# Kernel optimization log

Measured on AMD Instinct MI355X. Metric: run time of the kernel, lower is better.

The kernel has to match this reference:

```python
import jax, jax.numpy as jnp
import numpy as np

B, N, F = 4, 4096, 32
NG = 14  # number of gate graph-convs in GCNLSTM_Cell with memory state


def setup_inputs() -> dict:
    key = jax.random.key(0)
    ks = jax.random.split(key, 7)
    x = jax.random.normal(ks[0], (B, N, F), jnp.float32)
    h = jax.random.normal(ks[1], (B, N, F), jnp.float32)
    c = jax.random.normal(ks[2], (B, N, F), jnp.float32)
    m = jax.random.normal(ks[3], (B, N, F), jnp.float32)
    # weighted dense adjacency, scaled so row sums are O(1)
    adj = jax.random.uniform(ks[4], (N, N), jnp.float32) / N
    # 14 WeightedGraphConv layers: Dense F -> 2F (single FeedForward layer, no relu)
    W = jax.random.normal(ks[5], (NG, F, 2 * F), jnp.float32) * (1.0 / np.sqrt(F))
    b = jnp.zeros((NG, 2 * F), jnp.float32)
    return {"x": x, "h": h, "c": c, "m": m, "adj": adj, "W": W, "b": b}


def _gcn(ax, W, b):
    # ax: [B,N,F] = adj @ state (precomputed); Dense to 2F then GLU split.
    z = ax @ W + b  # [B,N,2F]
    ls, rs = jnp.split(z, 2, axis=-1)
    return ls * jax.nn.sigmoid(rs)


def reference(x, h, c, m, adj, W, b):
    # shared graph aggregation for x and h (adj is the same for all gates)
    ax = jnp.einsum('nm,bmf->bnf', adj, x)  # [B,N,F]
    ah = jnp.einsum('nm,bmf->bnf', adj, h)

    fx = _gcn(ax, W[0], b[0]); fh = _gcn(ah, W[1], b[1])
    ix = _gcn(ax, W[2], b[2]); ih = _gcn(ah, W[3], b[3])
    cx = _gcn(ax, W[4], b[4]); ch = _gcn(ah, W[5], b[5])
    ox = _gcn(ax, W[6], b[6]); oh = _gcn(ah, W[7], b[7])

    f = jax.nn.sigmoid(fx + fh)
    i = jax.nn.sigmoid(ix + ih)
    o = jax.nn.sigmoid(ox + oh)
    c_new = f * c + i * jnp.tanh(cx + ch)
    h1 = o * jnp.tanh(c_new)

    # memory-state block (6 more graph convs on h1 and m)
    ah1 = jnp.einsum('nm,bmf->bnf', adj, h1)
    am = jnp.einsum('nm,bmf->bnf', adj, m)
    sa_ih = _gcn(ah1, W[8], b[8]);  sa_im = _gcn(am, W[9], b[9])
    sa_gh = _gcn(ah1, W[10], b[10]); sa_gm = _gcn(am, W[11], b[11])
    sa_oh = _gcn(ah1, W[12], b[12]); sa_om = _gcn(am, W[13], b[13])

    i2 = jax.nn.sigmoid(sa_ih + sa_im)
    g = jax.nn.sigmoid(sa_gh + sa_gm)
    o2 = jax.nn.sigmoid(sa_oh + sa_om)
    m_new = i2 * m + (1.0 - i2) * g
    h_new = m_new * o2
    return h_new, c_new, m_new
```

## Files before the change

### kernel.cpp

```cpp
#include <hip/hip_runtime.h>
#include <stdint.h>

typedef __attribute__((ext_vector_type(4))) float f32x4;
typedef __attribute__((ext_vector_type(8))) short s16x8;

#define BB 4
#define NN 4096
#define FF 32
#define BNF (BB*NN*FF)

static __device__ __forceinline__ float bf2f(uint16_t u) {
    union { uint32_t i; float f; } v; v.i = ((uint32_t)u) << 16; return v.f;
}
static __device__ __forceinline__ uint16_t f2bf(float f) {
    union { float f; uint32_t i; } v; v.f = f;
    uint32_t r = v.i + 0x7FFFu + ((v.i >> 16) & 1u);
    return (uint16_t)(r >> 16);
}
static __device__ __forceinline__ float sig_acc(float x) { return 1.0f / (1.0f + expf(-x)); }

__global__ __launch_bounds__(256) void cvt_adj(const float* __restrict__ a,
                                               uint16_t* __restrict__ ab)
{
    size_t i = ((size_t)blockIdx.x * 256 + threadIdx.x) * 8;
    float4 v0 = *(const float4*)(a + i);
    float4 v1 = *(const float4*)(a + i + 4);
    union { uint4 u; uint16_t e[8]; } o;
    o.e[0] = f2bf(v0.x); o.e[1] = f2bf(v0.y); o.e[2] = f2bf(v0.z); o.e[3] = f2bf(v0.w);
    o.e[4] = f2bf(v1.x); o.e[5] = f2bf(v1.y); o.e[6] = f2bf(v1.z); o.e[7] = f2bf(v1.w);
    *(uint4*)(ab + i) = o.u;
}

__global__ __launch_bounds__(256) void prep_w(const float* __restrict__ Wf,
                                              uint16_t* __restrict__ Wp)
{
    int idx = blockIdx.x * 256 + threadIdx.x;
    int g   = idx >> 11;
    int k   = (idx >> 6) & 31;
    int col = idx & 63;
    uint16_t v = f2bf(Wf[idx]);
    int gp = g >> 1;
    int sl = ((g & 1) << 2) | (k >> 3);
    int ph = sl ^ (col & 7);
    Wp[((gp * 64 + col) * 64) + ph * 8 + (k & 7)] = v;
}

__global__ __launch_bounds__(256) void pack_kernel(
    const float* __restrict__ s0, const float* __restrict__ s1,
    uint16_t* __restrict__ dst)
{
    int bid = blockIdx.x;
    int tensor = bid >> 8;
    int b = (bid >> 6) & 3;
    int ntile = bid & 63;
    const float* src = tensor ? s1 : s0;
    int n0 = ntile * 64;
    __shared__ uint16_t tl[32][65];
    int t = threadIdx.x;
    {
        int i = t >> 2, ch = t & 3;
        size_t idx = ((size_t)(b * NN + n0 + i)) * FF + ch * 8;
        float4 v0 = *(const float4*)(src + idx);
        float4 v1 = *(const float4*)(src + idx + 4);
        uint16_t e[8] = { f2bf(v0.x), f2bf(v0.y), f2bf(v0.z), f2bf(v0.w),
                          f2bf(v1.x), f2bf(v1.y), f2bf(v1.z), f2bf(v1.w) };
        #pragma unroll
        for (int k = 0; k < 8; k++) tl[ch * 8 + k][i] = e[k];
    }
    __syncthreads();
    {
        int f = t >> 3, ch = t & 7;
        union { uint4 u; uint16_t e[8]; } v;
        #pragma unroll
        for (int k = 0; k < 8; k++) v.e[k] = tl[f][ch * 8 + k];
        size_t row = (size_t)(tensor * 128 + b * 32 + f);
        *(uint4*)(dst + row * NN + n0 + ch * 8) = v.u;
    }
}

__global__ __launch_bounds__(256) void gemm_kernel(
    const void* __restrict__ Av,
    const uint16_t* __restrict__ Bt,
    float* __restrict__ part, uint16_t* __restrict__ Cb,
    int kLen, int direct, int isf32A)
{
    int mt = blockIdx.x, nt = blockIdx.y, ks = blockIdx.z;
    int m0 = mt * 128, c0 = nt * 128, k0 = ks * kLen;
    __shared__ __align__(16) uint16_t aL[128 * 32];
    __shared__ __align__(16) uint16_t bL[128 * 32];
    int t = threadIdx.x;
    int lane = t & 63, w = t >> 6;
    int wm = (w & 1) * 64, wn = (w >> 1) * 64;
    int lm = lane & 15, lk = lane >> 4;

    const uint16_t* A16 = (const uint16_t*)Av;
    const float*    Af  = (const float*)Av;

    f32x4 acc[4][4] = {};

    for (int kk = k0; kk < k0 + kLen; kk += 32) {
        union { uint4 u; uint16_t e[8]; } sa[2], sb[2];
        #pragma unroll
        for (int q = 0; q < 2; q++) {
            int pos = q * 4096 + t * 16;
            int row = pos >> 6;
            int col = (pos & 63) >> 1;
            size_t aidx = (size_t)(m0 + row) * 4096 + kk + col;
            size_t bidx = (size_t)(c0 + row) * 4096 + kk + col;
            if (!isf32A) {
                sa[q].u = *(const uint4*)(A16 + aidx);
            } else {
                union { uint4 u[2]; float f[8]; } va;
                va.u[0] = *(const uint4*)(Af + aidx);
                va.u[1] = *(const uint4*)(Af + aidx + 4);
                #pragma unroll
                for (int k = 0; k < 8; k++) sa[q].e[k] = f2bf(va.f[k]);
            }
            sb[q].u = *(const uint4*)(Bt + bidx);
        }
        #pragma unroll
        for (int q = 0; q < 2; q++) {
            int pos = q * 4096 + t * 16;
            *(uint4*)((char*)aL + pos) = sa[q].u;
            *(uint4*)((char*)bL + pos) = sb[q].u;
        }
        __syncthreads();
        s16x8 af[4], bfr[4];
        #pragma unroll
        for (int i = 0; i < 4; i++)
            af[i] = *(const s16x8*)(aL + (wm + i * 16 + lm) * 32 + lk * 8);
        #pragma unroll
        for (int j = 0; j < 4; j++)
            bfr[j] = *(const s16x8*)(bL + (wn + j * 16 + lm) * 32 + lk * 8);
        #pragma unroll
        for (int i = 0; i < 4; i++)
            #pragma unroll
            for (int j = 0; j < 4; j++)
                acc[i][j] = __builtin_amdgcn_mfma_f32_16x16x32_bf16(af[i], bfr[j], acc[i][j], 0, 0, 0);
        __syncthreads();
    }

    int r4 = (lane >> 4) * 4;
    if (direct) {
        #pragma unroll
        for (int i = 0; i < 4; i++)
            #pragma unroll
            for (int j = 0; j < 4; j++) {
                int c = c0 + wn + j * 16 + lm;
                int mr = m0 + wm + i * 16 + r4;
                union { uint2 u; uint16_t e[4]; } v;
                #pragma unroll
                for (int r = 0; r < 4; r++) v.e[r] = f2bf(acc[i][j][r]);
                *(uint2*)(Cb + (size_t)c * 4096 + mr) = v.u;
            }
    } else {
        #pragma unroll
        for (int i = 0; i < 4; i++)
            #pragma unroll
            for (int j = 0; j < 4; j++) {
                int c = c0 + wn + j * 16 + lm;
                int mr = m0 + wm + i * 16 + r4;
                *(f32x4*)(part + ((size_t)ks * 256 + c) * 4096 + mr) = acc[i][j];
            }
    }
}

__global__ __launch_bounds__(256) void fuse1_kernel(
    const float* __restrict__ part,
    const uint16_t* __restrict__ Cbi,
    const uint16_t* __restrict__ Wp,
    const float* __restrict__ bf_,
    const float* __restrict__ cf,
    float* __restrict__ cnew, uint16_t* __restrict__ S2t, int ns)
{
    __shared__ __align__(16) uint16_t WL[4 * 64 * 64];
    __shared__ __align__(16) float    AL[64 * 68];
    __shared__ __align__(16) float    BL[512];
    __shared__ __align__(16) uint16_t H1[32 * 72];

    int t = threadIdx.x;
    int b = blockIdx.x >> 6, n0 = (blockIdx.x & 63) * 64;

    {
        const uint4* src = (const uint4*)Wp;
        uint4* dst = (uint4*)WL;
        #pragma unroll
        for (int i = 0; i < 8; i++) dst[t + i * 256] = src[t + i * 256];
    }
    if (t < 128) *(float4*)(BL + t * 4) = *(const float4*)(bf_ + t * 4);

    {
        int r = t >> 2, ch = t & 3;
        size_t crow = (r < 32) ? (size_t)(b * 32 + r) : (size_t)(128 + b * 32 + (r - 32));
        f32x4 a0, a1, a2, a3;
        if (ns) {
            const float* s0p = part + crow * 4096 + n0 + ch * 16;
            a0 = *(const f32x4*)(s0p);
            a1 = *(const f32x4*)(s0p + 4);
            a2 = *(const f32x4*)(s0p + 8);
            a3 = *(const f32x4*)(s0p + 12);
            for (int ks = 1; ks < ns; ks++) {
                const float* sp = s0p + (size_t)ks * (256 * 4096);
                a0 += *(const f32x4*)(sp);
                a1 += *(const f32x4*)(sp + 4);
                a2 += *(const f32x4*)(sp + 8);
                a3 += *(const f32x4*)(sp + 12);
            }
        } else {
            const uint16_t* cp = Cbi + crow * 4096 + n0 + ch * 16;
            union { uint4 u; uint16_t e[8]; } v0, v1;
            v0.u = *(const uint4*)(cp);
            v1.u = *(const uint4*)(cp + 8);
            #pragma unroll
            for (int k = 0; k < 4; k++) {
                a0[k] = bf2f(v0.e[k]);     a1[k] = bf2f(v0.e[4 + k]);
                a2[k] = bf2f(v1.e[k]);     a3[k] = bf2f(v1.e[4 + k]);
            }
        }
        float* al = AL + r * 68 + ch * 16;
        *(f32x4*)(al) = a0; *(f32x4*)(al + 4) = a1;
        *(f32x4*)(al + 8) = a2; *(f32x4*)(al + 12) = a3;
    }
    __syncthreads();

    int lane = t & 63, w = t >> 6;
    int j = lane & 15, kg = lane >> 4;
    int r4 = kg * 4;

    float cv[2][4];
    #pragma unroll
    for (int h = 0; h < 2; h++)
        #pragma unroll
        for (int r = 0; r < 4; r++)
            cv[h][r] = cf[((size_t)(b * NN + n0 + w * 16 + r4 + r)) * FF + j + h * 16];

    s16x8 a_ax, a_ah;
    {
        int col = w * 16 + j;
        #pragma unroll
        for (int e = 0; e < 8; e++) {
            int k = kg * 8 + e;
            a_ax[e] = (short)f2bf(AL[k * 68 + col]);
            a_ah[e] = (short)f2bf(AL[(32 + k) * 68 + col]);
        }
    }

    float s[4][2][4];
    #pragma unroll
    for (int p = 0; p < 4; p++) {
        int g0 = p * 2, g1 = p * 2 + 1;
        f32x4 ac0[4] = {}, ac1[4] = {};
        #pragma unroll
        for (int ct = 0; ct < 4; ct++) {
            int col = ct * 16 + j;
            int ph0 = (kg)     ^ (col & 7);
            int ph1 = (4 + kg) ^ (col & 7);
            s16x8 b0 = *(const s16x8*)(WL + (p * 64 + col) * 64 + ph0 * 8);
            s16x8 b1 = *(const s16x8*)(WL + (p * 64 + col) * 64 + ph1 * 8);
            ac0[ct] = __builtin_amdgcn_mfma_f32_16x16x32_bf16(a_ax, b0, ac0[ct], 0, 0, 0);
            ac1[ct] = __builtin_amdgcn_mfma_f32_16x16x32_bf16(a_ah, b1, ac1[ct], 0, 0, 0);
        }
        #pragma unroll
        for (int h = 0; h < 2; h++)
            #pragma unroll
            for (int r = 0; r < 4; r++) {
                float z0l = ac0[h][r]     + BL[g0 * 64 + h * 16 + j];
                float z0r = ac0[2 + h][r] + BL[g0 * 64 + 32 + h * 16 + j];
                float z1l = ac1[h][r]     + BL[g1 * 64 + h * 16 + j];
                float z1r = ac1[2 + h][r] + BL[g1 * 64 + 32 + h * 16 + j];
                s[p][h][r] = z0l * sig_acc(z0r) + z1l * sig_acc(z1r);
            }
    }

    #pragma unroll
    for (int h = 0; h < 2; h++) {
        union { uint2 u; uint16_t e[4]; } pk;
        #pragma unroll
        for (int r = 0; r < 4; r++) {
            size_t gidx = ((size_t)(b * NN + n0 + w * 16 + r4 + r)) * FF + j + h * 16;
            float fg = sig_acc(s[0][h][r]);
            float ig = sig_acc(s[1][h][r]);
            float cc = tanhf(s[2][h][r]);
            float og = sig_acc(s[3][h][r]);
            float cn = fg * cv[h][r] + ig * cc;
            cnew[gidx] = cn;
            pk.e[r] = f2bf(og * tanhf(cn));
        }
        *(uint2*)(H1 + (j + h * 16) * 72 + w * 16 + r4) = pk.u;
    }
    __syncthreads();
    {
        int fr = t >> 3, ch = t & 7;
        uint4 v = *(const uint4*)(H1 + fr * 72 + ch * 8);
        *(uint4*)(S2t + ((size_t)(b * 32 + fr)) * NN + n0 + ch * 8) = v;
    }
}

__global__ __launch_bounds__(256) void fuse2_kernel(
    const float* __restrict__ part,
    const uint16_t* __restrict__ Cbi,
    const uint16_t* __restrict__ Wp,
    const float* __restrict__ bf_,
    const float* __restrict__ mf,
    float* __restrict__ hnew, float* __restrict__ mnew, int ns)
{
    __shared__ __align__(16) uint16_t WL[3 * 64 * 64];
    __shared__ __align__(16) float    AL[64 * 68];
    __shared__ __align__(16) float    BL[384];

    int t = threadIdx.x;
    int b = blockIdx.x >> 6, n0 = (blockIdx.x & 63) * 64;

    {
        const uint4* src = (const uint4*)(Wp + 4 * 64 * 64);
        uint4* dst = (uint4*)WL;
        #pragma unroll
        for (int i = 0; i < 6; i++) dst[t + i * 256] = src[t + i * 256];
    }
    if (t < 96) *(float4*)(BL + t * 4) = *(const float4*)(bf_ + 512 + t * 4);

    {
        int r = t >> 2, ch = t & 3;
        size_t crow = (r < 32) ? (size_t)(b * 32 + r) : (size_t)(128 + b * 32 + (r - 32));
        f32x4 a0, a1, a2, a3;
        if (ns) {
            const float* s0p = part + crow * 4096 + n0 + ch * 16;
            a0 = *(const f32x4*)(s0p);
            a1 = *(const f32x4*)(s0p + 4);
            a2 = *(const f32x4*)(s0p + 8);
            a3 = *(const f32x4*)(s0p + 12);
            for (int ks = 1; ks < ns; ks++) {
                const float* sp = s0p + (size_t)ks * (256 * 4096);
                a0 += *(const f32x4*)(sp);
                a1 += *(const f32x4*)(sp + 4);
                a2 += *(const f32x4*)(sp + 8);
                a3 += *(const f32x4*)(sp + 12);
            }
        } else {
            const uint16_t* cp = Cbi + crow * 4096 + n0 + ch * 16;
            union { uint4 u; uint16_t e[8]; } v0, v1;
            v0.u = *(const uint4*)(cp);
            v1.u = *(const uint4*)(cp + 8);
            #pragma unroll
            for (int k = 0; k < 4; k++) {
                a0[k] = bf2f(v0.e[k]);     a1[k] = bf2f(v0.e[4 + k]);
                a2[k] = bf2f(v1.e[k]);     a3[k] = bf2f(v1.e[4 + k]);
            }
        }
        float* al = AL + r * 68 + ch * 16;
        *(f32x4*)(al) = a0; *(f32x4*)(al + 4) = a1;
        *(f32x4*)(al + 8) = a2; *(f32x4*)(al + 12) = a3;
    }
    __syncthreads();

    int lane = t & 63, w = t >> 6;
    int j = lane & 15, kg = lane >> 4;
    int r4 = kg * 4;

    float mv[2][4];
    #pragma unroll
    for (int h = 0; h < 2; h++)
        #pragma unroll
        for (int r = 0; r < 4; r++)
            mv[h][r] = mf[((size_t)(b * NN + n0 + w * 16 + r4 + r)) * FF + j + h * 16];

    s16x8 a_h1, a_m;
    {
        int col = w * 16 + j;
        #pragma unroll
        for (int e = 0; e < 8; e++) {
            int k = kg * 8 + e;
            a_h1[e] = (short)f2bf(AL[k * 68 + col]);
            a_m[e]  = (short)f2bf(AL[(32 + k) * 68 + col]);
        }
    }

    float s[3][2][4];
    #pragma unroll
    for (int p = 0; p < 3; p++) {
        int g0 = p * 2, g1 = p * 2 + 1;
        f32x4 ac0[4] = {}, ac1[4] = {};
        #pragma unroll
        for (int ct = 0; ct < 4; ct++) {
            int col = ct * 16 + j;
            int ph0 = (kg)     ^ (col & 7);
            int ph1 = (4 + kg) ^ (col & 7);
            s16x8 b0 = *(const s16x8*)(WL + (p * 64 + col) * 64 + ph0 * 8);
            s16x8 b1 = *(const s16x8*)(WL + (p * 64 + col) * 64 + ph1 * 8);
            ac0[ct] = __builtin_amdgcn_mfma_f32_16x16x32_bf16(a_h1, b0, ac0[ct], 0, 0, 0);
            ac1[ct] = __builtin_amdgcn_mfma_f32_16x16x32_bf16(a_m, b1, ac1[ct], 0, 0, 0);
        }
        #pragma unroll
        for (int h = 0; h < 2; h++)
            #pragma unroll
            for (int r = 0; r < 4; r++) {
                float z0l = ac0[h][r]     + BL[g0 * 64 + h * 16 + j];
                float z0r = ac0[2 + h][r] + BL[g0 * 64 + 32 + h * 16 + j];
                float z1l = ac1[h][r]     + BL[g1 * 64 + h * 16 + j];
                float z1r = ac1[2 + h][r] + BL[g1 * 64 + 32 + h * 16 + j];
                s[p][h][r] = z0l * sig_acc(z0r) + z1l * sig_acc(z1r);
            }
    }

    #pragma unroll
    for (int h = 0; h < 2; h++)
        #pragma unroll
        for (int r = 0; r < 4; r++) {
            size_t gidx = ((size_t)(b * NN + n0 + w * 16 + r4 + r)) * FF + j + h * 16;
            float i2 = sig_acc(s[0][h][r]);
            float gg = sig_acc(s[1][h][r]);
            float o2 = sig_acc(s[2][h][r]);
            float mn = i2 * mv[h][r] + (1.0f - i2) * gg;
            mnew[gidx] = mn;
            hnew[gidx] = mn * o2;
        }
}

extern "C" void kernel_launch(void* const* d_in, const int* in_sizes, int n_in,
                              void* d_out, int out_size, void* d_ws, size_t ws_size,
                              hipStream_t stream) {
    (void)in_sizes; (void)n_in; (void)out_size;
    const float* x   = (const float*)d_in[0];
    const float* h   = (const float*)d_in[1];
    const float* c   = (const float*)d_in[2];
    const float* m   = (const float*)d_in[3];
    const float* adj = (const float*)d_in[4];
    const float* W   = (const float*)d_in[5];
    const float* bb  = (const float*)d_in[6];
    float* out = (float*)d_out;

    char* ws = (char*)d_ws;
    int haveAdjb = ws_size >= (size_t)(40u << 20);
    uint16_t* adjb = (uint16_t*)ws;
    size_t pOff = haveAdjb ? (size_t)(32u << 20) : 0;
    uint16_t* P    = (uint16_t*)(ws + pOff);
    uint16_t* Cbuf = (uint16_t*)(ws + pOff + (2u << 20));
    uint16_t* Wp   = (uint16_t*)(ws + pOff + (4u << 20));
    size_t partOff = pOff + (5u << 20);
    float* part = (float*)(ws + partOff);

    if (ws_size < (6u << 20)) return;
    size_t avail = ws_size - partOff;
    int ns = 0;
    if      (avail >= (size_t)(32u << 20)) ns = 8;
    else if (avail >= (size_t)(16u << 20)) ns = 4;
    else if (avail >= (size_t)( 8u << 20)) ns = 2;
    else if (avail >= (size_t)( 4u << 20)) ns = 1;

    const void* Agemm = haveAdjb ? (const void*)adjb : (const void*)adj;
    int isf32A = haveAdjb ? 0 : 1;

    if (haveAdjb) cvt_adj<<<8192, 256, 0, stream>>>(adj, adjb);
    prep_w<<<112, 256, 0, stream>>>(W, Wp);

    pack_kernel<<<512, 256, 0, stream>>>(x, h, P);
    if (ns) {
        gemm_kernel<<<dim3(32, 2, ns), 256, 0, stream>>>(Agemm, P, part, nullptr, 4096 / ns, 0, isf32A);
    } else {
        gemm_kernel<<<dim3(32, 2, 1), 256, 0, stream>>>(Agemm, P, nullptr, Cbuf, 4096, 1, isf32A);
    }
    fuse1_kernel<<<256, 256, 0, stream>>>(part, Cbuf, Wp, bb, c, out + BNF, P, ns);
    pack_kernel<<<256, 256, 0, stream>>>(m, m, P + (size_t)128 * NN);
    if (ns) {
        gemm_kernel<<<dim3(32, 2, ns), 256, 0, stream>>>(Agemm, P, part, nullptr, 4096 / ns, 0, isf32A);
    } else {
        gemm_kernel<<<dim3(32, 2, 1), 256, 0, stream>>>(Agemm, P, nullptr, Cbuf, 4096, 1, isf32A);
    }
    fuse2_kernel<<<256, 256, 0, stream>>>(part, Cbuf, Wp, bb, m, out, out + 2 * BNF, ns);
}
```

Before: 186.2 us.

## Merge prep kernels into one launch and use direct global-to-LDS loads with swizzle

Folds the adjacency conversion, weight packing and all three state packs (x, h, m) into a single prep launch, which needs a separate P2 buffer so fuse1 no longer overwrites the packed m rows. The GEMM bf16 path now issues global_load_lds to write tiles straight into shared memory, skipping the register round trip. It also applies an XOR swizzle on the k-slot to reduce LDS bank conflicts on the fragment reads. The bf16 adjacency path now requires a larger workspace threshold, so with smaller workspaces the code falls back to the fp32 A path, which could be slower.

Result: faster. 180.5 us (-3.1%).

```diff
diff --git a/kernel.cpp b/kernel.cpp
--- a/kernel.cpp
+++ b/kernel.cpp
@@ -9,6 +9,9 @@
 #define FF 32
 #define BNF (BB*NN*FF)
 
+typedef __attribute__((address_space(3))) void       as3_void;
+typedef const __attribute__((address_space(1))) void as1_cvoid;
+
 static __device__ __forceinline__ float bf2f(uint16_t u) {
     union { uint32_t i; float f; } v; v.i = ((uint32_t)u) << 16; return v.f;
 }
@@ -19,44 +22,53 @@
 }
 static __device__ __forceinline__ float sig_acc(float x) { return 1.0f / (1.0f + expf(-x)); }
 
-__global__ __launch_bounds__(256) void cvt_adj(const float* __restrict__ a,
-                                               uint16_t* __restrict__ ab)
-{
-    size_t i = ((size_t)blockIdx.x * 256 + threadIdx.x) * 8;
-    float4 v0 = *(const float4*)(a + i);
-    float4 v1 = *(const float4*)(a + i + 4);
-    union { uint4 u; uint16_t e[8]; } o;
-    o.e[0] = f2bf(v0.x); o.e[1] = f2bf(v0.y); o.e[2] = f2bf(v0.z); o.e[3] = f2bf(v0.w);
-    o.e[4] = f2bf(v1.x); o.e[5] = f2bf(v1.y); o.e[6] = f2bf(v1.z); o.e[7] = f2bf(v1.w);
-    *(uint4*)(ab + i) = o.u;
-}
-
-__global__ __launch_bounds__(256) void prep_w(const float* __restrict__ Wf,
-                                              uint16_t* __restrict__ Wp)
-{
-    int idx = blockIdx.x * 256 + threadIdx.x;
-    int g   = idx >> 11;
-    int k   = (idx >> 6) & 31;
-    int col = idx & 63;
-    uint16_t v = f2bf(Wf[idx]);
-    int gp = g >> 1;
-    int sl = ((g & 1) << 2) | (k >> 3);
-    int ph = sl ^ (col & 7);
-    Wp[((gp * 64 + col) * 64) + ph * 8 + (k & 7)] = v;
-}
-
-__global__ __launch_bounds__(256) void pack_kernel(
-    const float* __restrict__ s0, const float* __restrict__ s1,
-    uint16_t* __restrict__ dst)
+__global__ __launch_bounds__(256) void prep_kernel(
+    const float* __restrict__ adj, uint16_t* __restrict__ adjb, int cvtN,
+    const float* __restrict__ Wf, uint16_t* __restrict__ Wp,
+    const float* __restrict__ x, const float* __restrict__ h,
+    const float* __restrict__ m,
+    uint16_t* __restrict__ P, uint16_t* __restrict__ P2)
 {
     int bid = blockIdx.x;
-    int tensor = bid >> 8;
-    int b = (bid >> 6) & 3;
-    int ntile = bid & 63;
-    const float* src = tensor ? s1 : s0;
-    int n0 = ntile * 64;
+    int t = threadIdx.x;
+
+    if (bid < cvtN) {
+        size_t i = ((size_t)bid * 256 + t) * 8;
+        float4 v0 = *(const float4*)(adj + i);
+        float4 v1 = *(const float4*)(adj + i + 4);
+        union { uint4 u; uint16_t e[8]; } o;
+        o.e[0] = f2bf(v0.x); o.e[1] = f2bf(v0.y); o.e[2] = f2bf(v0.z); o.e[3] = f2bf(v0.w);
+        o.e[4] = f2bf(v1.x); o.e[5] = f2bf(v1.y); o.e[6] = f2bf(v1.z); o.e[7] = f2bf(v1.w);
+        *(uint4*)(adjb + i) = o.u;
+        return;
+    }
+    bid -= cvtN;
+
+    if (bid < 112) {
+        int idx = bid * 256 + t;
+        int g   = idx >> 11;
+        int k   = (idx >> 6) & 31;
+        int col = idx & 63;
+        uint16_t v = f2bf(Wf[idx]);
+        int gp = g >> 1;
+        int sl = ((g & 1) << 2) | (k >> 3);
+        int ph = sl ^ (col & 7);
+        Wp[((gp * 64 + col) * 64) + ph * 8 + (k & 7)] = v;
+        return;
+    }
+    bid -= 112;
+
+    const float* src; uint16_t* dst; int rowbase, b, n0;
+    if (bid < 512) {
+        int tensor = bid >> 8;
+        src = tensor ? h : x; dst = P; rowbase = tensor * 128;
+        b = (bid >> 6) & 3; n0 = (bid & 63) * 64;
+    } else {
+        int q = bid - 512;
+        src = m; dst = P2; rowbase = 128;
+        b = q >> 6; n0 = (q & 63) * 64;
+    }
     __shared__ uint16_t tl[32][65];
-    int t = threadIdx.x;
     {
         int i = t >> 2, ch = t & 3;
         size_t idx = ((size_t)(b * NN + n0 + i)) * FF + ch * 8;
@@ -73,7 +85,7 @@
         union { uint4 u; uint16_t e[8]; } v;
         #pragma unroll
         for (int k = 0; k < 8; k++) v.e[k] = tl[f][ch * 8 + k];
-        size_t row = (size_t)(tensor * 128 + b * 32 + f);
+        size_t row = (size_t)(rowbase + b * 32 + f);
         *(uint4*)(dst + row * NN + n0 + ch * 8) = v.u;
     }
 }
@@ -99,39 +111,56 @@
     f32x4 acc[4][4] = {};
 
     for (int kk = k0; kk < k0 + kLen; kk += 32) {
-        union { uint4 u; uint16_t e[8]; } sa[2], sb[2];
-        #pragma unroll
-        for (int q = 0; q < 2; q++) {
-            int pos = q * 4096 + t * 16;
-            int row = pos >> 6;
-            int col = (pos & 63) >> 1;
-            size_t aidx = (size_t)(m0 + row) * 4096 + kk + col;
-            size_t bidx = (size_t)(c0 + row) * 4096 + kk + col;
-            if (!isf32A) {
-                sa[q].u = *(const uint4*)(A16 + aidx);
-            } else {
+        if (!isf32A) {
+            #pragma unroll
+            for (int q = 0; q < 2; q++) {
+                int pos  = q * 4096 + t * 16;
+                int row  = pos >> 6;
+                int slot = ((pos >> 4) & 3) ^ ((row >> 1) & 3);
+                int col  = slot * 8;
+                size_t aidx = (size_t)(m0 + row) * 4096 + kk + col;
+                size_t bidx = (size_t)(c0 + row) * 4096 + kk + col;
+                __builtin_amdgcn_global_load_lds((as1_cvoid*)(A16 + aidx),
+                                                 (as3_void*)((char*)aL + pos), 16, 0, 0);
+                __builtin_amdgcn_global_load_lds((as1_cvoid*)(Bt + bidx),
+                                                 (as3_void*)((char*)bL + pos), 16, 0, 0);
+            }
+        } else {
+            union { uint4 u; uint16_t e[8]; } sa[2], sb[2];
+            #pragma unroll
+            for (int q = 0; q < 2; q++) {
+                int pos  = q * 4096 + t * 16;
+                int row  = pos >> 6;
+                int slot = ((pos >> 4) & 3) ^ ((row >> 1) & 3);
+                int col  = slot * 8;
+                size_t aidx = (size_t)(m0 + row) * 4096 + kk + col;
+                size_t bidx = (size_t)(c0 + row) * 4096 + kk + col;
                 union { uint4 u[2]; float f[8]; } va;
                 va.u[0] = *(const uint4*)(Af + aidx);
                 va.u[1] = *(const uint4*)(Af + aidx + 4);
                 #pragma unroll
                 for (int k = 0; k < 8; k++) sa[q].e[k] = f2bf(va.f[k]);
-            }
-            sb[q].u = *(const uint4*)(Bt + bidx);
-        }
-        #pragma unroll
-        for (int q = 0; q < 2; q++) {
-            int pos = q * 4096 + t * 16;
-            *(uint4*)((char*)aL + pos) = sa[q].u;
-            *(uint4*)((char*)bL + pos) = sb[q].u;
+                sb[q].u = *(const uint4*)(Bt + bidx);
+            }
+            #pragma unroll
+            for (int q = 0; q < 2; q++) {
+                int pos = q * 4096 + t * 16;
+                *(uint4*)((char*)aL + pos) = sa[q].u;
+                *(uint4*)((char*)bL + pos) = sb[q].u;
+            }
         }
         __syncthreads();
         s16x8 af[4], bfr[4];
         #pragma unroll
-        for (int i = 0; i < 4; i++)
-            af[i] = *(const s16x8*)(aL + (wm + i * 16 + lm) * 32 + lk * 8);
-        #pragma unroll
-        for (int j = 0; j < 4; j++)
-            bfr[j] = *(const s16x8*)(bL + (wn + j * 16 + lm) * 32 + lk * 8);
+        for (int i = 0; i < 4; i++) {
+            int r = wm + i * 16 + lm;
+            af[i] = *(const s16x8*)(aL + r * 32 + ((lk ^ ((r >> 1) & 3)) * 8));
+        }
+        #pragma unroll
+        for (int j = 0; j < 4; j++) {
+            int r = wn + j * 16 + lm;
+            bfr[j] = *(const s16x8*)(bL + r * 32 + ((lk ^ ((r >> 1) & 3)) * 8));
+        }
         #pragma unroll
         for (int i = 0; i < 4; i++)
             #pragma unroll
@@ -430,16 +459,17 @@
     float* out = (float*)d_out;
 
     char* ws = (char*)d_ws;
-    int haveAdjb = ws_size >= (size_t)(40u << 20);
+    int haveAdjb = ws_size >= (size_t)(72u << 20);
     uint16_t* adjb = (uint16_t*)ws;
     size_t pOff = haveAdjb ? (size_t)(32u << 20) : 0;
     uint16_t* P    = (uint16_t*)(ws + pOff);
-    uint16_t* Cbuf = (uint16_t*)(ws + pOff + (2u << 20));
-    uint16_t* Wp   = (uint16_t*)(ws + pOff + (4u << 20));
-    size_t partOff = pOff + (5u << 20);
+    uint16_t* P2   = (uint16_t*)(ws + pOff + (2u << 20));
+    uint16_t* Cbuf = (uint16_t*)(ws + pOff + (4u << 20));
+    uint16_t* Wp   = (uint16_t*)(ws + pOff + (6u << 20));
+    size_t partOff = pOff + (7u << 20);
     float* part = (float*)(ws + partOff);
 
-    if (ws_size < (6u << 20)) return;
+    if (ws_size < (8u << 20)) return;
     size_t avail = ws_size - partOff;
     int ns = 0;
     if      (avail >= (size_t)(32u << 20)) ns = 8;
@@ -449,22 +479,20 @@
 
     const void* Agemm = haveAdjb ? (const void*)adjb : (const void*)adj;
     int isf32A = haveAdjb ? 0 : 1;
-
-    if (haveAdjb) cvt_adj<<<8192, 256, 0, stream>>>(adj, adjb);
-    prep_w<<<112, 256, 0, stream>>>(W, Wp);
-
-    pack_kernel<<<512, 256, 0, stream>>>(x, h, P);
+    int cvtN = haveAdjb ? 8192 : 0;
+
+    prep_kernel<<<cvtN + 112 + 768, 256, 0, stream>>>(adj, adjb, cvtN, W, Wp, x, h, m, P, P2);
+
     if (ns) {
         gemm_kernel<<<dim3(32, 2, ns), 256, 0, stream>>>(Agemm, P, part, nullptr, 4096 / ns, 0, isf32A);
     } else {
         gemm_kernel<<<dim3(32, 2, 1), 256, 0, stream>>>(Agemm, P, nullptr, Cbuf, 4096, 1, isf32A);
     }
-    fuse1_kernel<<<256, 256, 0, stream>>>(part, Cbuf, Wp, bb, c, out + BNF, P, ns);
-    pack_kernel<<<256, 256, 0, stream>>>(m, m, P + (size_t)128 * NN);
+    fuse1_kernel<<<256, 256, 0, stream>>>(part, Cbuf, Wp, bb, c, out + BNF, P2, ns);
     if (ns) {
-        gemm_kernel<<<dim3(32, 2, ns), 256, 0, stream>>>(Agemm, P, part, nullptr, 4096 / ns, 0, isf32A);
+        gemm_kernel<<<dim3(32, 2, ns), 256, 0, stream>>>(Agemm, P2, part, nullptr, 4096 / ns, 0, isf32A);
     } else {
-        gemm_kernel<<<dim3(32, 2, 1), 256, 0, stream>>>(Agemm, P, nullptr, Cbuf, 4096, 1, isf32A);
+        gemm_kernel<<<dim3(32, 2, 1), 256, 0, stream>>>(Agemm, P2, nullptr, Cbuf, 4096, 1, isf32A);
     }
     fuse2_kernel<<<256, 256, 0, stream>>>(part, Cbuf, Wp, bb, m, out, out + 2 * BNF, ns);
 }
```
